# Performance work log

Measured on AMD Instinct MI355X. Metric: run time of the kernel, lower is better.

Reference implementation:

```python
import jax, jax.numpy as jnp
import numpy as np

D = 2048   # input_size = hidden1 = hidden2 = output_size
MH = 32    # meta_weight hidden size (3 -> MH -> 1 MLP with ReLU)


def setup_inputs() -> dict:
    key = jax.random.key(0)
    ks = jax.random.split(key, 8)
    def lin(k, out_d, in_d):
        return jax.random.normal(k, (out_d, in_d), jnp.float32) / np.float32(np.sqrt(in_d))
    return {
        "x": jax.random.normal(ks[0], (1, D), jnp.float32),
        "W1": lin(ks[1], D, D), "b1": jnp.zeros((D,), jnp.float32),
        "W2": lin(ks[2], D, D), "b2": jnp.zeros((D,), jnp.float32),
        "W3": lin(ks[3], D, D), "b3": jnp.zeros((D,), jnp.float32),
        "Wm1": jax.random.normal(ks[4], (3, MH), jnp.float32) / np.float32(np.sqrt(3.0)),
        "bm1": jnp.zeros((MH,), jnp.float32),
        "Wm2": jax.random.normal(ks[5], (MH, 1), jnp.float32) / np.float32(np.sqrt(MH)),
        "bm2": jnp.zeros((1,), jnp.float32),
    }


def _meta_update(W, inp, outp, Wm1, bm1, Wm2, bm2):
    # W: [O, I] (torch Linear weight layout), inp: [1, I] pre-layer activation,
    # outp: [1, O] post-layer activation. meta_inputs[o, i] = (v_i, w_oi, v_o),
    # matching torch.stack((input_stack, layer, output_stack), dim=2).
    O, I = W.shape
    mi = jnp.stack(
        [jnp.broadcast_to(inp[0][None, :], (O, I)),
         W,
         jnp.broadcast_to(outp[0][:, None], (O, I))],
        axis=-1)                                   # [O, I, 3]
    h = jax.nn.relu(jnp.einsum("oik,km->oim", mi, Wm1) + bm1)  # [O, I, MH]
    new_w = jnp.einsum("oim,mn->oin", h, Wm2)[..., 0] + bm2[0]  # [O, I]
    return new_w


def reference(x, W1, b1, W2, b2, W3, b3, Wm1, bm1, Wm2, bm2):
    # 3-layer MLP forward (ReLU after every layer, including the last)
    a0 = x
    a1 = jax.nn.relu(a0 @ W1.T + b1)
    a2 = jax.nn.relu(a1 @ W2.T + b2)
    out = jax.nn.relu(a2 @ W3.T + b3)
    # Vectorized per-weight meta-network updates (replaces the nested Python
    # double for-loop over hidden1*hidden2 scalar meta_weight.forward calls).
    # Updates read original activations/weights, so they are order-independent.
    nW1 = _meta_update(W1, a0, a1, Wm1, bm1, Wm2, bm2)
    nW2 = _meta_update(W2, a1, a2, Wm1, bm1, Wm2, bm2)
    nW3 = _meta_update(W3, a2, out, Wm1, bm1, Wm2, bm2)
    return out, nW1, nW2, nW3
```

## Files before the change

kernel.cpp:

```cpp
#include <hip/hip_runtime.h>

#define DD 2048
#define MHH 32

typedef _Float16 hf2 __attribute__((ext_vector_type(2)));

__device__ __forceinline__ unsigned pack_pair(float lo, float hi) {
    hf2 v;
    v.x = (_Float16)lo;
    v.y = (_Float16)hi;
    return __builtin_bit_cast(unsigned, v);
}

__device__ __forceinline__ hf2 rfl2(unsigned u) {
    u = __builtin_amdgcn_readfirstlane(u);
    return __builtin_bit_cast(hf2, u);
}

__device__ __forceinline__ hf2 dup16(float x) {
    hf2 v;
    v.x = (_Float16)x;
    v.y = v.x;
    return v;
}

__device__ __forceinline__ void gemv4_body(const float* __restrict__ W,
                                           const float* __restrict__ x,
                                           const float* __restrict__ b,
                                           float* __restrict__ y, int blk) {
    const int wave = threadIdx.x >> 6;
    const int lane = threadIdx.x & 63;
    const int row  = (blk << 2) + wave;
    const float* Wr = W + (size_t)row * DD;
    float acc = 0.f;
#pragma unroll
    for (int it = 0; it < 8; ++it) {
        const int col = ((it << 6) + lane) << 2;
        const float4 w4 = *reinterpret_cast<const float4*>(Wr + col);
        const float4 x4 = *reinterpret_cast<const float4*>(x + col);
        acc = fmaf(w4.x, x4.x, acc);
        acc = fmaf(w4.y, x4.y, acc);
        acc = fmaf(w4.z, x4.z, acc);
        acc = fmaf(w4.w, x4.w, acc);
    }
#pragma unroll
    for (int off = 32; off > 0; off >>= 1)
        acc += __shfl_down(acc, off, 64);
    if (lane == 0) {
        const float v = acc + b[row];
        y[row] = fmaxf(v, 0.f);
    }
}

__global__ __launch_bounds__(256) void gemv_relu_prep_k(const float* __restrict__ W,
                                                        const float* __restrict__ x,
                                                        const float* __restrict__ b,
                                                        float* __restrict__ y,
                                                        const float* __restrict__ Wm1,
                                                        const float* __restrict__ bm1,
                                                        const float* __restrict__ Wm2,
                                                        unsigned* __restrict__ cst) {
    if (blockIdx.x == DD / 4) {
        const int mp = threadIdx.x;
        if (mp < MHH / 2) {
            const int m = 2 * mp;
            cst[mp]      = pack_pair(Wm1[m],           Wm1[m + 1]);
            cst[16 + mp] = pack_pair(Wm1[MHH + m],     Wm1[MHH + m + 1]);
            cst[32 + mp] = pack_pair(Wm2[m],           Wm2[m + 1]);
            cst[48 + mp] = pack_pair(Wm1[2 * MHH + m], Wm1[2 * MHH + m + 1]);
            cst[64 + mp] = pack_pair(bm1[m],           bm1[m + 1]);
        }
        return;
    }
    gemv4_body(W, x, b, y, blockIdx.x);
}

__global__ __launch_bounds__(256) void gemv_relu_k(const float* __restrict__ W,
                                                   const float* __restrict__ x,
                                                   const float* __restrict__ b,
                                                   float* __restrict__ y) {
    gemv4_body(W, x, b, y, blockIdx.x);
}

__global__ __launch_bounds__(256, 6) void meta_k(const float* __restrict__ W1,
                                                 const float* __restrict__ W2,
                                                 const float* __restrict__ W3,
                                                 const float* __restrict__ a0,
                                                 const float* __restrict__ a1,
                                                 const float* __restrict__ a2,
                                                 const float* __restrict__ a3,
                                                 const unsigned* __restrict__ cst,
                                                 const float* __restrict__ bm2,
                                                 float* __restrict__ nW) {
    const int layer = blockIdx.x >> 9;
    const int row0  = (blockIdx.x & 511) << 2;

    const float* W   = (layer == 0) ? W1 : (layer == 1) ? W2 : W3;
    const float* inp = (layer == 0) ? a0 : (layer == 1) ? a1 : a2;
    const float* oup = (layer == 0) ? a1 : (layer == 1) ? a2 : a3;

    const float* Wr  = W  + (size_t)row0 * DD;
    float*       nWr = nW + (size_t)layer * DD * DD + (size_t)row0 * DD;

    const int col0 = threadIdx.x * 4;
    const int col1 = (DD / 2) + threadIdx.x * 4;

    const float4 u4a = *reinterpret_cast<const float4*>(inp + col0);
    const float4 u4b = *reinterpret_cast<const float4*>(inp + col1);
    const float4 ov4 = *reinterpret_cast<const float4*>(oup + row0);

    const uint4* c16 = (const uint4*)cst;
    hf2 Ap[MHH / 2], Bp[MHH / 2], Vp[MHH / 2], Cm[MHH / 2], Bm[MHH / 2];
#pragma unroll
    for (int j = 0; j < 4; ++j) {
        const uint4 t = c16[j];
        Ap[4 * j + 0] = rfl2(t.x); Ap[4 * j + 1] = rfl2(t.y);
        Ap[4 * j + 2] = rfl2(t.z); Ap[4 * j + 3] = rfl2(t.w);
    }
#pragma unroll
    for (int j = 0; j < 4; ++j) {
        const uint4 t = c16[4 + j];
        Bp[4 * j + 0] = rfl2(t.x); Bp[4 * j + 1] = rfl2(t.y);
        Bp[4 * j + 2] = rfl2(t.z); Bp[4 * j + 3] = rfl2(t.w);
    }
#pragma unroll
    for (int j = 0; j < 4; ++j) {
        const uint4 t = c16[8 + j];
        Vp[4 * j + 0] = rfl2(t.x); Vp[4 * j + 1] = rfl2(t.y);
        Vp[4 * j + 2] = rfl2(t.z); Vp[4 * j + 3] = rfl2(t.w);
    }
#pragma unroll
    for (int j = 0; j < 4; ++j) {
        const uint4 tc = c16[12 + j];
        const uint4 tb = c16[16 + j];
        Cm[4 * j + 0] = rfl2(tc.x); Cm[4 * j + 1] = rfl2(tc.y);
        Cm[4 * j + 2] = rfl2(tc.z); Cm[4 * j + 3] = rfl2(tc.w);
        Bm[4 * j + 0] = __builtin_bit_cast(hf2, tb.x);
        Bm[4 * j + 1] = __builtin_bit_cast(hf2, tb.y);
        Bm[4 * j + 2] = __builtin_bit_cast(hf2, tb.z);
        Bm[4 * j + 3] = __builtin_bit_cast(hf2, tb.w);
    }
    const float bias2 = bm2[0];

    hf2 ud[8];
    ud[0] = dup16(u4a.x); ud[1] = dup16(u4a.y); ud[2] = dup16(u4a.z); ud[3] = dup16(u4a.w);
    ud[4] = dup16(u4b.x); ud[5] = dup16(u4b.y); ud[6] = dup16(u4b.z); ud[7] = dup16(u4b.w);
    asm volatile("" : "+v"(ud[0]), "+v"(ud[1]), "+v"(ud[2]), "+v"(ud[3]),
                      "+v"(ud[4]), "+v"(ud[5]), "+v"(ud[6]), "+v"(ud[7]));

    const hf2 zero = (hf2)(_Float16)0.f;

#pragma unroll
    for (int r = 0; r < 4; ++r) {
        const float* Wrr = Wr + (size_t)r * DD;
        const float4 wa = *reinterpret_cast<const float4*>(Wrr + col0);
        const float4 wb = *reinterpret_cast<const float4*>(Wrr + col1);
        const float ovr = (r == 0) ? ov4.x : (r == 1) ? ov4.y : (r == 2) ? ov4.z : ov4.w;
        const hf2 ovd = dup16(ovr);

        hf2 Pp[MHH / 2];
#pragma unroll
        for (int mp = 0; mp < MHH / 2; ++mp) {
            Pp[mp] = __builtin_elementwise_fma(ovd, Cm[mp], Bm[mp]);
            asm volatile("" : "+v"(Pp[mp]));
        }

        hf2 wd[8];
        wd[0] = dup16(wa.x); wd[1] = dup16(wa.y); wd[2] = dup16(wa.z); wd[3] = dup16(wa.w);
        wd[4] = dup16(wb.x); wd[5] = dup16(wb.y); wd[6] = dup16(wb.z); wd[7] = dup16(wb.w);

        float c0 = bias2, c1 = bias2, c2 = bias2, c3 = bias2;
        float c4 = bias2, c5 = bias2, c6 = bias2, c7 = bias2;

#pragma unroll
        for (int mp = 0; mp < MHH / 2; ++mp) {
            const hf2 a = Ap[mp], b = Bp[mp], v = Vp[mp], p = Pp[mp];
            hf2 q0 = __builtin_elementwise_fma(ud[0], a, p);
            hf2 q1 = __builtin_elementwise_fma(ud[1], a, p);
            hf2 q2 = __builtin_elementwise_fma(ud[2], a, p);
            hf2 q3 = __builtin_elementwise_fma(ud[3], a, p);
            hf2 q4 = __builtin_elementwise_fma(ud[4], a, p);
            hf2 q5 = __builtin_elementwise_fma(ud[5], a, p);
            hf2 q6 = __builtin_elementwise_fma(ud[6], a, p);
            hf2 q7 = __builtin_elementwise_fma(ud[7], a, p);
            q0 = __builtin_elementwise_fma(wd[0], b, q0);
            q1 = __builtin_elementwise_fma(wd[1], b, q1);
            q2 = __builtin_elementwise_fma(wd[2], b, q2);
            q3 = __builtin_elementwise_fma(wd[3], b, q3);
            q4 = __builtin_elementwise_fma(wd[4], b, q4);
            q5 = __builtin_elementwise_fma(wd[5], b, q5);
            q6 = __builtin_elementwise_fma(wd[6], b, q6);
            q7 = __builtin_elementwise_fma(wd[7], b, q7);
            q0 = __builtin_elementwise_max(q0, zero);
            q1 = __builtin_elementwise_max(q1, zero);
            q2 = __builtin_elementwise_max(q2, zero);
            q3 = __builtin_elementwise_max(q3, zero);
            q4 = __builtin_elementwise_max(q4, zero);
            q5 = __builtin_elementwise_max(q5, zero);
            q6 = __builtin_elementwise_max(q6, zero);
            q7 = __builtin_elementwise_max(q7, zero);
            c0 = __builtin_amdgcn_fdot2(q0, v, c0, false);
            c1 = __builtin_amdgcn_fdot2(q1, v, c1, false);
            c2 = __builtin_amdgcn_fdot2(q2, v, c2, false);
            c3 = __builtin_amdgcn_fdot2(q3, v, c3, false);
            c4 = __builtin_amdgcn_fdot2(q4, v, c4, false);
            c5 = __builtin_amdgcn_fdot2(q5, v, c5, false);
            c6 = __builtin_amdgcn_fdot2(q6, v, c6, false);
            c7 = __builtin_amdgcn_fdot2(q7, v, c7, false);
        }

        float4 r0, r1;
        r0.x = c0; r0.y = c1; r0.z = c2; r0.w = c3;
        r1.x = c4; r1.y = c5; r1.z = c6; r1.w = c7;
        float* nWrr = nWr + (size_t)r * DD;
        *reinterpret_cast<float4*>(nWrr + col0) = r0;
        *reinterpret_cast<float4*>(nWrr + col1) = r1;
    }
}

extern "C" void kernel_launch(void* const* d_in, const int* in_sizes, int n_in,
                              void* d_out, int out_size, void* d_ws, size_t ws_size,
                              hipStream_t stream) {
    const float* x   = (const float*)d_in[0];
    const float* W1  = (const float*)d_in[1];
    const float* b1  = (const float*)d_in[2];
    const float* W2  = (const float*)d_in[3];
    const float* b2  = (const float*)d_in[4];
    const float* W3  = (const float*)d_in[5];
    const float* b3  = (const float*)d_in[6];
    const float* Wm1 = (const float*)d_in[7];
    const float* bm1 = (const float*)d_in[8];
    const float* Wm2 = (const float*)d_in[9];
    const float* bm2 = (const float*)d_in[10];

    float* out = (float*)d_out;
    float* nW  = out + DD;
    float* a1  = (float*)d_ws;
    float* a2  = a1 + DD;
    unsigned* cst = (unsigned*)(a2 + DD);

    gemv_relu_prep_k<<<DD / 4 + 1, 256, 0, stream>>>(W1, x, b1, a1, Wm1, bm1, Wm2, cst);
    gemv_relu_k<<<DD / 4, 256, 0, stream>>>(W2, a1, b2, a2);
    gemv_relu_k<<<DD / 4, 256, 0, stream>>>(W3, a2, b3, out);
    meta_k<<<3 * DD / 4, 256, 0, stream>>>(W1, W2, W3, x, a1, a2, out,
                                           cst, bm2, nW);
}
```

Measured before the change: 45.61 us.

## Restructure meta kernel to 512-thread blocks with shared per-row P terms in LDS

The meta-update kernel now uses 512 threads per block, each covering 4 columns instead of 8, and processes 8 rows per block instead of 4. The per-row output-dependent term (ov*Wm1[2]+bm1) is computed once per block into shared memory rather than in registers by every thread, which removes the Cm/Bm register arrays and the per-row FMA loop. The intent is to cut redundant ALU work and register pressure so occupancy rises. The cost is a block-wide barrier, LDS reads on every row, and half as much instruction-level parallelism per thread in the inner loop.

```diff
diff --git a/kernel.cpp b/kernel.cpp
--- a/kernel.cpp
+++ b/kernel.cpp
@@ -82,7 +82,7 @@
     gemv4_body(W, x, b, y, blockIdx.x);
 }
 
-__global__ __launch_bounds__(256, 6) void meta_k(const float* __restrict__ W1,
+__global__ __launch_bounds__(512, 6) void meta_k(const float* __restrict__ W1,
                                                  const float* __restrict__ W2,
                                                  const float* __restrict__ W3,
                                                  const float* __restrict__ a0,
@@ -92,8 +92,8 @@
                                                  const unsigned* __restrict__ cst,
                                                  const float* __restrict__ bm2,
                                                  float* __restrict__ nW) {
-    const int layer = blockIdx.x >> 9;
-    const int row0  = (blockIdx.x & 511) << 2;
+    const int layer = blockIdx.x >> 8;
+    const int row0  = (blockIdx.x & 255) << 3;
 
     const float* W   = (layer == 0) ? W1 : (layer == 1) ? W2 : W3;
     const float* inp = (layer == 0) ? a0 : (layer == 1) ? a1 : a2;
@@ -102,15 +102,23 @@
     const float* Wr  = W  + (size_t)row0 * DD;
     float*       nWr = nW + (size_t)layer * DD * DD + (size_t)row0 * DD;
 
-    const int col0 = threadIdx.x * 4;
-    const int col1 = (DD / 2) + threadIdx.x * 4;
-
-    const float4 u4a = *reinterpret_cast<const float4*>(inp + col0);
-    const float4 u4b = *reinterpret_cast<const float4*>(inp + col1);
-    const float4 ov4 = *reinterpret_cast<const float4*>(oup + row0);
+    const int col = threadIdx.x * 4;
+
+    const float4 u4 = *reinterpret_cast<const float4*>(inp + col);
+
+    __shared__ __align__(16) unsigned Plds[8 * 16];
+    if (threadIdx.x < 128) {
+        const int r  = threadIdx.x >> 4;
+        const int mp = threadIdx.x & 15;
+        const hf2 ovd = dup16(oup[row0 + r]);
+        const hf2 Cv  = __builtin_bit_cast(hf2, cst[48 + mp]);
+        const hf2 Bv  = __builtin_bit_cast(hf2, cst[64 + mp]);
+        const hf2 p   = __builtin_elementwise_fma(ovd, Cv, Bv);
+        Plds[r * 16 + mp] = __builtin_bit_cast(unsigned, p);
+    }
 
     const uint4* c16 = (const uint4*)cst;
-    hf2 Ap[MHH / 2], Bp[MHH / 2], Vp[MHH / 2], Cm[MHH / 2], Bm[MHH / 2];
+    hf2 Ap[MHH / 2], Bp[MHH / 2], Vp[MHH / 2];
 #pragma unroll
     for (int j = 0; j < 4; ++j) {
         const uint4 t = c16[j];
@@ -129,48 +137,39 @@
         Vp[4 * j + 0] = rfl2(t.x); Vp[4 * j + 1] = rfl2(t.y);
         Vp[4 * j + 2] = rfl2(t.z); Vp[4 * j + 3] = rfl2(t.w);
     }
-#pragma unroll
-    for (int j = 0; j < 4; ++j) {
-        const uint4 tc = c16[12 + j];
-        const uint4 tb = c16[16 + j];
-        Cm[4 * j + 0] = rfl2(tc.x); Cm[4 * j + 1] = rfl2(tc.y);
-        Cm[4 * j + 2] = rfl2(tc.z); Cm[4 * j + 3] = rfl2(tc.w);
-        Bm[4 * j + 0] = __builtin_bit_cast(hf2, tb.x);
-        Bm[4 * j + 1] = __builtin_bit_cast(hf2, tb.y);
-        Bm[4 * j + 2] = __builtin_bit_cast(hf2, tb.z);
-        Bm[4 * j + 3] = __builtin_bit_cast(hf2, tb.w);
-    }
     const float bias2 = bm2[0];
 
-    hf2 ud[8];
-    ud[0] = dup16(u4a.x); ud[1] = dup16(u4a.y); ud[2] = dup16(u4a.z); ud[3] = dup16(u4a.w);
-    ud[4] = dup16(u4b.x); ud[5] = dup16(u4b.y); ud[6] = dup16(u4b.z); ud[7] = dup16(u4b.w);
-    asm volatile("" : "+v"(ud[0]), "+v"(ud[1]), "+v"(ud[2]), "+v"(ud[3]),
-                      "+v"(ud[4]), "+v"(ud[5]), "+v"(ud[6]), "+v"(ud[7]));
+    hf2 ud[4];
+    ud[0] = dup16(u4.x); ud[1] = dup16(u4.y); ud[2] = dup16(u4.z); ud[3] = dup16(u4.w);
+    asm volatile("" : "+v"(ud[0]), "+v"(ud[1]), "+v"(ud[2]), "+v"(ud[3]));
 
     const hf2 zero = (hf2)(_Float16)0.f;
 
-#pragma unroll
-    for (int r = 0; r < 4; ++r) {
+    __syncthreads();
+
+#pragma unroll
+    for (int r = 0; r < 8; ++r) {
         const float* Wrr = Wr + (size_t)r * DD;
-        const float4 wa = *reinterpret_cast<const float4*>(Wrr + col0);
-        const float4 wb = *reinterpret_cast<const float4*>(Wrr + col1);
-        const float ovr = (r == 0) ? ov4.x : (r == 1) ? ov4.y : (r == 2) ? ov4.z : ov4.w;
-        const hf2 ovd = dup16(ovr);
-
-        hf2 Pp[MHH / 2];
-#pragma unroll
-        for (int mp = 0; mp < MHH / 2; ++mp) {
-            Pp[mp] = __builtin_elementwise_fma(ovd, Cm[mp], Bm[mp]);
-            asm volatile("" : "+v"(Pp[mp]));
+        const float4 wa = *reinterpret_cast<const float4*>(Wrr + col);
+
+        const uint4* pl = (const uint4*)&Plds[r * 16];
+        hf2 Pp[16];
+#pragma unroll
+        for (int j = 0; j < 4; ++j) {
+            const uint4 t = pl[j];
+            Pp[4 * j + 0] = __builtin_bit_cast(hf2, t.x);
+            Pp[4 * j + 1] = __builtin_bit_cast(hf2, t.y);
+            Pp[4 * j + 2] = __builtin_bit_cast(hf2, t.z);
+            Pp[4 * j + 3] = __builtin_bit_cast(hf2, t.w);
+            asm volatile("" : "+v"(Pp[4 * j + 0]), "+v"(Pp[4 * j + 1]),
+                              "+v"(Pp[4 * j + 2]), "+v"(Pp[4 * j + 3]));
         }
 
-        hf2 wd[8];
+        hf2 wd[4];
         wd[0] = dup16(wa.x); wd[1] = dup16(wa.y); wd[2] = dup16(wa.z); wd[3] = dup16(wa.w);
-        wd[4] = dup16(wb.x); wd[5] = dup16(wb.y); wd[6] = dup16(wb.z); wd[7] = dup16(wb.w);
+        asm volatile("" : "+v"(wd[0]), "+v"(wd[1]), "+v"(wd[2]), "+v"(wd[3]));
 
         float c0 = bias2, c1 = bias2, c2 = bias2, c3 = bias2;
-        float c4 = bias2, c5 = bias2, c6 = bias2, c7 = bias2;
 
 #pragma unroll
         for (int mp = 0; mp < MHH / 2; ++mp) {
@@ -179,42 +178,23 @@
             hf2 q1 = __builtin_elementwise_fma(ud[1], a, p);
             hf2 q2 = __builtin_elementwise_fma(ud[2], a, p);
             hf2 q3 = __builtin_elementwise_fma(ud[3], a, p);
-            hf2 q4 = __builtin_elementwise_fma(ud[4], a, p);
-            hf2 q5 = __builtin_elementwise_fma(ud[5], a, p);
-            hf2 q6 = __builtin_elementwise_fma(ud[6], a, p);
-            hf2 q7 = __builtin_elementwise_fma(ud[7], a, p);
             q0 = __builtin_elementwise_fma(wd[0], b, q0);
             q1 = __builtin_elementwise_fma(wd[1], b, q1);
             q2 = __builtin_elementwise_fma(wd[2], b, q2);
             q3 = __builtin_elementwise_fma(wd[3], b, q3);
-            q4 = __builtin_elementwise_fma(wd[4], b, q4);
-            q5 = __builtin_elementwise_fma(wd[5], b, q5);
-            q6 = __builtin_elementwise_fma(wd[6], b, q6);
-            q7 = __builtin_elementwise_fma(wd[7], b, q7);
             q0 = __builtin_elementwise_max(q0, zero);
             q1 = __builtin_elementwise_max(q1, zero);
             q2 = __builtin_elementwise_max(q2, zero);
             q3 = __builtin_elementwise_max(q3, zero);
-            q4 = __builtin_elementwise_max(q4, zero);
-            q5 = __builtin_elementwise_max(q5, zero);
-            q6 = __builtin_elementwise_max(q6, zero);
-            q7 = __builtin_elementwise_max(q7, zero);
             c0 = __builtin_amdgcn_fdot2(q0, v, c0, false);
             c1 = __builtin_amdgcn_fdot2(q1, v, c1, false);
             c2 = __builtin_amdgcn_fdot2(q2, v, c2, false);
             c3 = __builtin_amdgcn_fdot2(q3, v, c3, false);
-            c4 = __builtin_amdgcn_fdot2(q4, v, c4, false);
-            c5 = __builtin_amdgcn_fdot2(q5, v, c5, false);
-            c6 = __builtin_amdgcn_fdot2(q6, v, c6, false);
-            c7 = __builtin_amdgcn_fdot2(q7, v, c7, false);
         }
 
-        float4 r0, r1;
-        r0.x = c0; r0.y = c1; r0.z = c2; r0.w = c3;
-        r1.x = c4; r1.y = c5; r1.z = c6; r1.w = c7;
-        float* nWrr = nWr + (size_t)r * DD;
-        *reinterpret_cast<float4*>(nWrr + col0) = r0;
-        *reinterpret_cast<float4*>(nWrr + col1) = r1;
+        float4 rr;
+        rr.x = c0; rr.y = c1; rr.z = c2; rr.w = c3;
+        *reinterpret_cast<float4*>(nWr + (size_t)r * DD + col) = rr;
     }
 }
 
@@ -242,6 +222,6 @@
     gemv_relu_prep_k<<<DD / 4 + 1, 256, 0, stream>>>(W1, x, b1, a1, Wm1, bm1, Wm2, cst);
     gemv_relu_k<<<DD / 4, 256, 0, stream>>>(W2, a1, b2, a2);
     gemv_relu_k<<<DD / 4, 256, 0, stream>>>(W3, a2, b3, out);
-    meta_k<<<3 * DD / 4, 256, 0, stream>>>(W1, W2, W3, x, a1, a2, out,
+    meta_k<<<3 * DD / 8, 512, 0, stream>>>(W1, W2, W3, x, a1, a2, out,
                                            cst, bm2, nW);
 }
```

Result: slower. 46.66 us (+2.3%).

## Fuse each layer's GEMV with its meta-weight update into one kernel

Applied to the files above, without the earlier changes.

Replaces the three separate GEMV kernels plus one combined meta-update kernel with a tiny prep kernel and three fused per-layer kernels. Each fused block computes two output rows of the GEMV, reduces them through shared memory, and reuses the same loaded weight rows to compute the meta-updated weights. This avoids reading each weight matrix from memory twice. The trade-off is that layers run serially, each meta update waits on the previous layer's activation, and only 1024 blocks per launch are available, with a block barrier and lower occupancy bounds.

```diff
diff --git a/kernel.cpp b/kernel.cpp
--- a/kernel.cpp
+++ b/kernel.cpp
@@ -24,90 +24,62 @@
     return v;
 }
 
-__device__ __forceinline__ void gemv4_body(const float* __restrict__ W,
-                                           const float* __restrict__ x,
-                                           const float* __restrict__ b,
-                                           float* __restrict__ y, int blk) {
+__global__ void prep_k(const float* __restrict__ Wm1, const float* __restrict__ bm1,
+                       const float* __restrict__ Wm2, unsigned* __restrict__ cst) {
+    const int mp = threadIdx.x;
+    if (mp < MHH / 2) {
+        const int m = 2 * mp;
+        cst[mp]      = pack_pair(Wm1[m],           Wm1[m + 1]);
+        cst[16 + mp] = pack_pair(Wm1[MHH + m],     Wm1[MHH + m + 1]);
+        cst[32 + mp] = pack_pair(Wm2[m],           Wm2[m + 1]);
+        cst[48 + mp] = pack_pair(Wm1[2 * MHH + m], Wm1[2 * MHH + m + 1]);
+        cst[64 + mp] = pack_pair(bm1[m],           bm1[m + 1]);
+    }
+}
+
+__global__ __launch_bounds__(256, 4) void fused_k(const float* __restrict__ W,
+                                                  const float* __restrict__ b,
+                                                  const float* __restrict__ inp,
+                                                  float* __restrict__ outp,
+                                                  const unsigned* __restrict__ cst,
+                                                  const float* __restrict__ bm2,
+                                                  float* __restrict__ nWl) {
+    const int row0 = blockIdx.x << 1;
     const int wave = threadIdx.x >> 6;
     const int lane = threadIdx.x & 63;
-    const int row  = (blk << 2) + wave;
-    const float* Wr = W + (size_t)row * DD;
-    float acc = 0.f;
-#pragma unroll
-    for (int it = 0; it < 8; ++it) {
-        const int col = ((it << 6) + lane) << 2;
-        const float4 w4 = *reinterpret_cast<const float4*>(Wr + col);
-        const float4 x4 = *reinterpret_cast<const float4*>(x + col);
-        acc = fmaf(w4.x, x4.x, acc);
-        acc = fmaf(w4.y, x4.y, acc);
-        acc = fmaf(w4.z, x4.z, acc);
-        acc = fmaf(w4.w, x4.w, acc);
-    }
-#pragma unroll
-    for (int off = 32; off > 0; off >>= 1)
-        acc += __shfl_down(acc, off, 64);
-    if (lane == 0) {
-        const float v = acc + b[row];
-        y[row] = fmaxf(v, 0.f);
-    }
-}
-
-__global__ __launch_bounds__(256) void gemv_relu_prep_k(const float* __restrict__ W,
-                                                        const float* __restrict__ x,
-                                                        const float* __restrict__ b,
-                                                        float* __restrict__ y,
-                                                        const float* __restrict__ Wm1,
-                                                        const float* __restrict__ bm1,
-                                                        const float* __restrict__ Wm2,
-                                                        unsigned* __restrict__ cst) {
-    if (blockIdx.x == DD / 4) {
-        const int mp = threadIdx.x;
-        if (mp < MHH / 2) {
-            const int m = 2 * mp;
-            cst[mp]      = pack_pair(Wm1[m],           Wm1[m + 1]);
-            cst[16 + mp] = pack_pair(Wm1[MHH + m],     Wm1[MHH + m + 1]);
-            cst[32 + mp] = pack_pair(Wm2[m],           Wm2[m + 1]);
-            cst[48 + mp] = pack_pair(Wm1[2 * MHH + m], Wm1[2 * MHH + m + 1]);
-            cst[64 + mp] = pack_pair(bm1[m],           bm1[m + 1]);
-        }
-        return;
-    }
-    gemv4_body(W, x, b, y, blockIdx.x);
-}
-
-__global__ __launch_bounds__(256) void gemv_relu_k(const float* __restrict__ W,
-                                                   const float* __restrict__ x,
-                                                   const float* __restrict__ b,
-                                                   float* __restrict__ y) {
-    gemv4_body(W, x, b, y, blockIdx.x);
-}
-
-__global__ __launch_bounds__(256, 6) void meta_k(const float* __restrict__ W1,
-                                                 const float* __restrict__ W2,
-                                                 const float* __restrict__ W3,
-                                                 const float* __restrict__ a0,
-                                                 const float* __restrict__ a1,
-                                                 const float* __restrict__ a2,
-                                                 const float* __restrict__ a3,
-                                                 const unsigned* __restrict__ cst,
-                                                 const float* __restrict__ bm2,
-                                                 float* __restrict__ nW) {
-    const int layer = blockIdx.x >> 9;
-    const int row0  = (blockIdx.x & 511) << 2;
-
-    const float* W   = (layer == 0) ? W1 : (layer == 1) ? W2 : W3;
-    const float* inp = (layer == 0) ? a0 : (layer == 1) ? a1 : a2;
-    const float* oup = (layer == 0) ? a1 : (layer == 1) ? a2 : a3;
-
-    const float* Wr  = W  + (size_t)row0 * DD;
-    float*       nWr = nW + (size_t)layer * DD * DD + (size_t)row0 * DD;
+
+    const float* Wr0 = W + (size_t)row0 * DD;
+    const float* Wr1 = Wr0 + DD;
+    float* nWr0 = nWl + (size_t)row0 * DD;
+    float* nWr1 = nWr0 + DD;
 
     const int col0 = threadIdx.x * 4;
     const int col1 = (DD / 2) + threadIdx.x * 4;
 
     const float4 u4a = *reinterpret_cast<const float4*>(inp + col0);
     const float4 u4b = *reinterpret_cast<const float4*>(inp + col1);
-    const float4 ov4 = *reinterpret_cast<const float4*>(oup + row0);
+    const float4 w0a = *reinterpret_cast<const float4*>(Wr0 + col0);
+    const float4 w0b = *reinterpret_cast<const float4*>(Wr0 + col1);
+    const float4 w1a = *reinterpret_cast<const float4*>(Wr1 + col0);
+    const float4 w1b = *reinterpret_cast<const float4*>(Wr1 + col1);
+    const float2 bb  = *reinterpret_cast<const float2*>(b + row0);
+
+    float p0 = 0.f, p1 = 0.f;
+    p0 = fmaf(w0a.x, u4a.x, p0); p0 = fmaf(w0a.y, u4a.y, p0);
+    p0 = fmaf(w0a.z, u4a.z, p0); p0 = fmaf(w0a.w, u4a.w, p0);
+    p0 = fmaf(w0b.x, u4b.x, p0); p0 = fmaf(w0b.y, u4b.y, p0);
+    p0 = fmaf(w0b.z, u4b.z, p0); p0 = fmaf(w0b.w, u4b.w, p0);
+    p1 = fmaf(w1a.x, u4a.x, p1); p1 = fmaf(w1a.y, u4a.y, p1);
+    p1 = fmaf(w1a.z, u4a.z, p1); p1 = fmaf(w1a.w, u4a.w, p1);
+    p1 = fmaf(w1b.x, u4b.x, p1); p1 = fmaf(w1b.y, u4b.y, p1);
+    p1 = fmaf(w1b.z, u4b.z, p1); p1 = fmaf(w1b.w, u4b.w, p1);
+#pragma unroll
+    for (int off = 32; off > 0; off >>= 1) {
+        p0 += __shfl_down(p0, off, 64);
+        p1 += __shfl_down(p1, off, 64);
+    }
+    __shared__ float red[4][2];
+    if (lane == 0) { red[wave][0] = p0; red[wave][1] = p1; }
 
     const uint4* c16 = (const uint4*)cst;
     hf2 Ap[MHH / 2], Bp[MHH / 2], Vp[MHH / 2], Cm[MHH / 2], Bm[MHH / 2];
@@ -148,16 +120,29 @@
     asm volatile("" : "+v"(ud[0]), "+v"(ud[1]), "+v"(ud[2]), "+v"(ud[3]),
                       "+v"(ud[4]), "+v"(ud[5]), "+v"(ud[6]), "+v"(ud[7]));
 
+    __syncthreads();
+    const float ov0 = fmaxf(red[0][0] + red[1][0] + red[2][0] + red[3][0] + bb.x, 0.f);
+    const float ov1 = fmaxf(red[0][1] + red[1][1] + red[2][1] + red[3][1] + bb.y, 0.f);
+    if (threadIdx.x == 0) {
+        outp[row0]     = ov0;
+        outp[row0 + 1] = ov1;
+    }
+
     const hf2 zero = (hf2)(_Float16)0.f;
 
 #pragma unroll
-    for (int r = 0; r < 4; ++r) {
-        const float* Wrr = Wr + (size_t)r * DD;
-        const float4 wa = *reinterpret_cast<const float4*>(Wrr + col0);
-        const float4 wb = *reinterpret_cast<const float4*>(Wrr + col1);
-        const float ovr = (r == 0) ? ov4.x : (r == 1) ? ov4.y : (r == 2) ? ov4.z : ov4.w;
+    for (int r = 0; r < 2; ++r) {
+        const float4 wa = r ? w1a : w0a;
+        const float4 wb = r ? w1b : w0b;
+        const float ovr = r ? ov1 : ov0;
+
+        hf2 wd[8];
+        wd[0] = dup16(wa.x); wd[1] = dup16(wa.y); wd[2] = dup16(wa.z); wd[3] = dup16(wa.w);
+        wd[4] = dup16(wb.x); wd[5] = dup16(wb.y); wd[6] = dup16(wb.z); wd[7] = dup16(wb.w);
+        asm volatile("" : "+v"(wd[0]), "+v"(wd[1]), "+v"(wd[2]), "+v"(wd[3]),
+                          "+v"(wd[4]), "+v"(wd[5]), "+v"(wd[6]), "+v"(wd[7]));
+
         const hf2 ovd = dup16(ovr);
-
         hf2 Pp[MHH / 2];
 #pragma unroll
         for (int mp = 0; mp < MHH / 2; ++mp) {
@@ -165,16 +150,12 @@
             asm volatile("" : "+v"(Pp[mp]));
         }
 
-        hf2 wd[8];
-        wd[0] = dup16(wa.x); wd[1] = dup16(wa.y); wd[2] = dup16(wa.z); wd[3] = dup16(wa.w);
-        wd[4] = dup16(wb.x); wd[5] = dup16(wb.y); wd[6] = dup16(wb.z); wd[7] = dup16(wb.w);
-
         float c0 = bias2, c1 = bias2, c2 = bias2, c3 = bias2;
         float c4 = bias2, c5 = bias2, c6 = bias2, c7 = bias2;
 
 #pragma unroll
         for (int mp = 0; mp < MHH / 2; ++mp) {
-            const hf2 a = Ap[mp], b = Bp[mp], v = Vp[mp], p = Pp[mp];
+            const hf2 a = Ap[mp], bq = Bp[mp], v = Vp[mp], p = Pp[mp];
             hf2 q0 = __builtin_elementwise_fma(ud[0], a, p);
             hf2 q1 = __builtin_elementwise_fma(ud[1], a, p);
             hf2 q2 = __builtin_elementwise_fma(ud[2], a, p);
@@ -183,14 +164,14 @@
             hf2 q5 = __builtin_elementwise_fma(ud[5], a, p);
             hf2 q6 = __builtin_elementwise_fma(ud[6], a, p);
             hf2 q7 = __builtin_elementwise_fma(ud[7], a, p);
-            q0 = __builtin_elementwise_fma(wd[0], b, q0);
-            q1 = __builtin_elementwise_fma(wd[1], b, q1);
-            q2 = __builtin_elementwise_fma(wd[2], b, q2);
-            q3 = __builtin_elementwise_fma(wd[3], b, q3);
-            q4 = __builtin_elementwise_fma(wd[4], b, q4);
-            q5 = __builtin_elementwise_fma(wd[5], b, q5);
-            q6 = __builtin_elementwise_fma(wd[6], b, q6);
-            q7 = __builtin_elementwise_fma(wd[7], b, q7);
+            q0 = __builtin_elementwise_fma(wd[0], bq, q0);
+            q1 = __builtin_elementwise_fma(wd[1], bq, q1);
+            q2 = __builtin_elementwise_fma(wd[2], bq, q2);
+            q3 = __builtin_elementwise_fma(wd[3], bq, q3);
+            q4 = __builtin_elementwise_fma(wd[4], bq, q4);
+            q5 = __builtin_elementwise_fma(wd[5], bq, q5);
+            q6 = __builtin_elementwise_fma(wd[6], bq, q6);
+            q7 = __builtin_elementwise_fma(wd[7], bq, q7);
             q0 = __builtin_elementwise_max(q0, zero);
             q1 = __builtin_elementwise_max(q1, zero);
             q2 = __builtin_elementwise_max(q2, zero);
@@ -209,12 +190,12 @@
             c7 = __builtin_amdgcn_fdot2(q7, v, c7, false);
         }
 
-        float4 r0, r1;
-        r0.x = c0; r0.y = c1; r0.z = c2; r0.w = c3;
-        r1.x = c4; r1.y = c5; r1.z = c6; r1.w = c7;
-        float* nWrr = nWr + (size_t)r * DD;
-        *reinterpret_cast<float4*>(nWrr + col0) = r0;
-        *reinterpret_cast<float4*>(nWrr + col1) = r1;
+        float4 r0v, r1v;
+        r0v.x = c0; r0v.y = c1; r0v.z = c2; r0v.w = c3;
+        r1v.x = c4; r1v.y = c5; r1v.z = c6; r1v.w = c7;
+        float* nWr = r ? nWr1 : nWr0;
+        *reinterpret_cast<float4*>(nWr + col0) = r0v;
+        *reinterpret_cast<float4*>(nWr + col1) = r1v;
     }
 }
 
@@ -234,14 +215,15 @@
     const float* bm2 = (const float*)d_in[10];
 
     float* out = (float*)d_out;
-    float* nW  = out + DD;
+    float* nW1 = out + DD;
+    float* nW2 = nW1 + (size_t)DD * DD;
+    float* nW3 = nW2 + (size_t)DD * DD;
     float* a1  = (float*)d_ws;
     float* a2  = a1 + DD;
     unsigned* cst = (unsigned*)(a2 + DD);
 
-    gemv_relu_prep_k<<<DD / 4 + 1, 256, 0, stream>>>(W1, x, b1, a1, Wm1, bm1, Wm2, cst);
-    gemv_relu_k<<<DD / 4, 256, 0, stream>>>(W2, a1, b2, a2);
-    gemv_relu_k<<<DD / 4, 256, 0, stream>>>(W3, a2, b3, out);
-    meta_k<<<3 * DD / 4, 256, 0, stream>>>(W1, W2, W3, x, a1, a2, out,
-                                           cst, bm2, nW);
-}
+    prep_k<<<1, 64, 0, stream>>>(Wm1, bm1, Wm2, cst);
+    fused_k<<<DD / 2, 256, 0, stream>>>(W1, b1, x,  a1,  cst, bm2, nW1);
+    fused_k<<<DD / 2, 256, 0, stream>>>(W2, b2, a1, a2,  cst, bm2, nW2);
+    fused_k<<<DD / 2, 256, 0, stream>>>(W3, b3, a2, out, cst, bm2, nW3);
+}
```

Result: slower. 51.79 us (+13.6%).

## Fuse layer-3 GEMV into meta kernel and recompute output activations in-block

Applied to the files above, without the earlier changes.

Merges the third GEMV launch into the meta-update kernel: the first 512 blocks compute the final layer output while the remaining blocks do meta updates. Each meta block now recomputes its own rows' post-activation values from the W rows it already loads, using a wave shuffle reduction plus a shared-memory sum, so it no longer depends on the previous layer's output being written. This removes one kernel launch and the dependency between launches, at the cost of extra FMAs, four __syncthreads per block, and fp32 recompute that may differ slightly in rounding from the GEMV result.

```diff
diff --git a/kernel.cpp b/kernel.cpp
--- a/kernel.cpp
+++ b/kernel.cpp
@@ -82,32 +82,45 @@
     gemv4_body(W, x, b, y, blockIdx.x);
 }
 
-__global__ __launch_bounds__(256, 6) void meta_k(const float* __restrict__ W1,
+__global__ __launch_bounds__(256, 6) void mega_k(const float* __restrict__ W3g,
+                                                 const float* __restrict__ b3g,
+                                                 const float* __restrict__ a2g,
+                                                 float* __restrict__ outg,
+                                                 const float* __restrict__ W1,
                                                  const float* __restrict__ W2,
                                                  const float* __restrict__ W3,
+                                                 const float* __restrict__ b1,
+                                                 const float* __restrict__ b2,
+                                                 const float* __restrict__ b3,
                                                  const float* __restrict__ a0,
                                                  const float* __restrict__ a1,
                                                  const float* __restrict__ a2,
-                                                 const float* __restrict__ a3,
                                                  const unsigned* __restrict__ cst,
                                                  const float* __restrict__ bm2,
                                                  float* __restrict__ nW) {
-    const int layer = blockIdx.x >> 9;
-    const int row0  = (blockIdx.x & 511) << 2;
+    if (blockIdx.x < DD / 4) {
+        gemv4_body(W3g, a2g, b3g, outg, blockIdx.x);
+        return;
+    }
+    const int bid   = blockIdx.x - DD / 4;
+    const int layer = bid >> 9;
+    const int row0  = (bid & 511) << 2;
 
     const float* W   = (layer == 0) ? W1 : (layer == 1) ? W2 : W3;
     const float* inp = (layer == 0) ? a0 : (layer == 1) ? a1 : a2;
-    const float* oup = (layer == 0) ? a1 : (layer == 1) ? a2 : a3;
+    const float* bv  = (layer == 0) ? b1 : (layer == 1) ? b2 : b3;
 
     const float* Wr  = W  + (size_t)row0 * DD;
     float*       nWr = nW + (size_t)layer * DD * DD + (size_t)row0 * DD;
 
+    const int wave = threadIdx.x >> 6;
+    const int lane = threadIdx.x & 63;
     const int col0 = threadIdx.x * 4;
     const int col1 = (DD / 2) + threadIdx.x * 4;
 
     const float4 u4a = *reinterpret_cast<const float4*>(inp + col0);
     const float4 u4b = *reinterpret_cast<const float4*>(inp + col1);
-    const float4 ov4 = *reinterpret_cast<const float4*>(oup + row0);
+    const float4 b4  = *reinterpret_cast<const float4*>(bv + row0);
 
     const uint4* c16 = (const uint4*)cst;
     hf2 Ap[MHH / 2], Bp[MHH / 2], Vp[MHH / 2], Cm[MHH / 2], Bm[MHH / 2];
@@ -149,15 +162,32 @@
                       "+v"(ud[4]), "+v"(ud[5]), "+v"(ud[6]), "+v"(ud[7]));
 
     const hf2 zero = (hf2)(_Float16)0.f;
+    __shared__ float red[4][4];
 
 #pragma unroll
     for (int r = 0; r < 4; ++r) {
         const float* Wrr = Wr + (size_t)r * DD;
         const float4 wa = *reinterpret_cast<const float4*>(Wrr + col0);
         const float4 wb = *reinterpret_cast<const float4*>(Wrr + col1);
-        const float ovr = (r == 0) ? ov4.x : (r == 1) ? ov4.y : (r == 2) ? ov4.z : ov4.w;
+
+        float p = 0.f;
+        p = fmaf(wa.x, u4a.x, p); p = fmaf(wa.y, u4a.y, p);
+        p = fmaf(wa.z, u4a.z, p); p = fmaf(wa.w, u4a.w, p);
+        p = fmaf(wb.x, u4b.x, p); p = fmaf(wb.y, u4b.y, p);
+        p = fmaf(wb.z, u4b.z, p); p = fmaf(wb.w, u4b.w, p);
+#pragma unroll
+        for (int off = 32; off > 0; off >>= 1)
+            p += __shfl_down(p, off, 64);
+        if (lane == 0) red[wave][r] = p;
+        __syncthreads();
+        const float br = (r == 0) ? b4.x : (r == 1) ? b4.y : (r == 2) ? b4.z : b4.w;
+        const float ovr = fmaxf(red[0][r] + red[1][r] + red[2][r] + red[3][r] + br, 0.f);
+
+        hf2 wd[8];
+        wd[0] = dup16(wa.x); wd[1] = dup16(wa.y); wd[2] = dup16(wa.z); wd[3] = dup16(wa.w);
+        wd[4] = dup16(wb.x); wd[5] = dup16(wb.y); wd[6] = dup16(wb.z); wd[7] = dup16(wb.w);
+
         const hf2 ovd = dup16(ovr);
-
         hf2 Pp[MHH / 2];
 #pragma unroll
         for (int mp = 0; mp < MHH / 2; ++mp) {
@@ -165,24 +195,20 @@
             asm volatile("" : "+v"(Pp[mp]));
         }
 
-        hf2 wd[8];
-        wd[0] = dup16(wa.x); wd[1] = dup16(wa.y); wd[2] = dup16(wa.z); wd[3] = dup16(wa.w);
-        wd[4] = dup16(wb.x); wd[5] = dup16(wb.y); wd[6] = dup16(wb.z); wd[7] = dup16(wb.w);
-
         float c0 = bias2, c1 = bias2, c2 = bias2, c3 = bias2;
         float c4 = bias2, c5 = bias2, c6 = bias2, c7 = bias2;
 
 #pragma unroll
         for (int mp = 0; mp < MHH / 2; ++mp) {
-            const hf2 a = Ap[mp], b = Bp[mp], v = Vp[mp], p = Pp[mp];
-            hf2 q0 = __builtin_elementwise_fma(ud[0], a, p);
-            hf2 q1 = __builtin_elementwise_fma(ud[1], a, p);
-            hf2 q2 = __builtin_elementwise_fma(ud[2], a, p);
-            hf2 q3 = __builtin_elementwise_fma(ud[3], a, p);
-            hf2 q4 = __builtin_elementwise_fma(ud[4], a, p);
-            hf2 q5 = __builtin_elementwise_fma(ud[5], a, p);
-            hf2 q6 = __builtin_elementwise_fma(ud[6], a, p);
-            hf2 q7 = __builtin_elementwise_fma(ud[7], a, p);
+            const hf2 a = Ap[mp], b = Bp[mp], v = Vp[mp], pq = Pp[mp];
+            hf2 q0 = __builtin_elementwise_fma(ud[0], a, pq);
+            hf2 q1 = __builtin_elementwise_fma(ud[1], a, pq);
+            hf2 q2 = __builtin_elementwise_fma(ud[2], a, pq);
+            hf2 q3 = __builtin_elementwise_fma(ud[3], a, pq);
+            hf2 q4 = __builtin_elementwise_fma(ud[4], a, pq);
+            hf2 q5 = __builtin_elementwise_fma(ud[5], a, pq);
+            hf2 q6 = __builtin_elementwise_fma(ud[6], a, pq);
+            hf2 q7 = __builtin_elementwise_fma(ud[7], a, pq);
             q0 = __builtin_elementwise_fma(wd[0], b, q0);
             q1 = __builtin_elementwise_fma(wd[1], b, q1);
             q2 = __builtin_elementwise_fma(wd[2], b, q2);
@@ -241,7 +267,7 @@
 
     gemv_relu_prep_k<<<DD / 4 + 1, 256, 0, stream>>>(W1, x, b1, a1, Wm1, bm1, Wm2, cst);
     gemv_relu_k<<<DD / 4, 256, 0, stream>>>(W2, a1, b2, a2);
-    gemv_relu_k<<<DD / 4, 256, 0, stream>>>(W3, a2, b3, out);
-    meta_k<<<3 * DD / 4, 256, 0, stream>>>(W1, W2, W3, x, a1, a2, out,
-                                           cst, bm2, nW);
-}
+    mega_k<<<DD / 4 + 3 * DD / 4, 256, 0, stream>>>(W3, b3, a2, out,
+                                                    W1, W2, W3, b1, b2, b3,
+                                                    x, a1, a2, cst, bm2, nW);
+}
```

Result: no change. 46.22 us (+1.3%).
